# Kernel optimization log

Measured on AMD Instinct MI355X. Metric: run time of the kernel, lower is better.

## Reference

```python
import jax, jax.numpy as jnp
import numpy as np

N, E, F_IN, HID, HEADS, CLS = 50000, 600000, 128, 128, 4, 10
OUT_PER_HEAD = HID // HEADS  # 32
NEG_SLOPE = 0.2
BN_EPS = 1e-5


def _gat_conv(h, src, dst, W, att_src, att_dst, bias, heads, out_dim, concat, num_nodes):
    # h: [N, in]; W: [in, heads*out]; att_*: [heads, out]; src/dst include self-loops
    hp = (h @ W).reshape(num_nodes, heads, out_dim)          # [N, H, D]
    a_s = jnp.sum(hp * att_src[None], axis=-1)               # [N, H]
    a_d = jnp.sum(hp * att_dst[None], axis=-1)               # [N, H]
    alpha = jax.nn.leaky_relu(a_s[src] + a_d[dst], NEG_SLOPE)  # [E, H]
    m = jax.ops.segment_max(alpha, dst, num_segments=num_nodes)
    m = jnp.where(jnp.isfinite(m), m, 0.0)
    ex = jnp.exp(alpha - m[dst])
    denom = jax.ops.segment_sum(ex, dst, num_segments=num_nodes)
    attn = ex / (denom[dst] + 1e-16)                         # segment softmax over dst
    msg = hp[src] * attn[..., None]                          # [E, H, D]
    out = jax.ops.segment_sum(msg, dst, num_segments=num_nodes)  # [N, H, D]
    out = out.reshape(num_nodes, heads * out_dim) if concat else out.mean(axis=1)
    return out + bias


def _bn_eval(x, gamma, beta):
    # eval-mode BatchNorm1d with running_mean=0, running_var=1
    return x * (gamma / jnp.sqrt(1.0 + BN_EPS)) + beta


def setup_inputs() -> dict:
    key = jax.random.key(0)
    ks = jax.random.split(key, 16)
    x = jax.random.normal(ks[0], (N, F_IN), dtype=jnp.float32)
    edge_index = jax.random.randint(ks[1], (2, E), 0, N, dtype=jnp.int64)
    s = 0.1
    return {
        "x": x,
        "edge_index": edge_index,
        "W0": jax.random.normal(ks[2], (F_IN, HID), jnp.float32) * s,
        "as0": jax.random.normal(ks[3], (HEADS, OUT_PER_HEAD), jnp.float32) * s,
        "ad0": jax.random.normal(ks[4], (HEADS, OUT_PER_HEAD), jnp.float32) * s,
        "b0": jnp.zeros((HID,), jnp.float32),
        "g0": jnp.ones((HID,), jnp.float32),
        "be0": jnp.zeros((HID,), jnp.float32),
        "W1": jax.random.normal(ks[5], (HID, HID), jnp.float32) * s,
        "as1": jax.random.normal(ks[6], (HEADS, OUT_PER_HEAD), jnp.float32) * s,
        "ad1": jax.random.normal(ks[7], (HEADS, OUT_PER_HEAD), jnp.float32) * s,
        "b1": jnp.zeros((HID,), jnp.float32),
        "g1": jnp.ones((HID,), jnp.float32),
        "be1": jnp.zeros((HID,), jnp.float32),
        "W2": jax.random.normal(ks[8], (HID, CLS), jnp.float32) * s,
        "as2": jax.random.normal(ks[9], (1, CLS), jnp.float32) * s,
        "ad2": jax.random.normal(ks[10], (1, CLS), jnp.float32) * s,
        "b2": jnp.zeros((CLS,), jnp.float32),
    }


def reference(x, edge_index, W0, as0, ad0, b0, g0, be0,
              W1, as1, ad1, b1, g1, be1, W2, as2, ad2, b2):
    # add self-loops (PyG GATConv default)
    loop = jnp.arange(N, dtype=edge_index.dtype)
    src = jnp.concatenate([edge_index[0], loop])
    dst = jnp.concatenate([edge_index[1], loop])
    h = _gat_conv(x, src, dst, W0, as0, ad0, b0, HEADS, OUT_PER_HEAD, True, N)
    h = jax.nn.elu(_bn_eval(h, g0, be0))
    h = _gat_conv(h, src, dst, W1, as1, ad1, b1, HEADS, OUT_PER_HEAD, True, N)
    h = jax.nn.elu(_bn_eval(h, g1, be1))
    out = _gat_conv(h, src, dst, W2, as2, ad2, b2, 1, CLS, False, N)
    return out
```

## Files before the change

### kernel.cpp

```cpp
#include <hip/hip_runtime.h>
#include <hip/hip_bf16.h>
#include <hip/hip_fp16.h>
#include <math.h>

#define N_NODES 50000
#define N_EDGES 600000
#define E_TOT   (N_EDGES + N_NODES)
#define F       128
#define HEADS   4
#define DHEAD   32
#define CLS     10
#define CLS_PAD 16


__global__ void count_deg(const int* __restrict__ ei, int* __restrict__ deg) {
    int e = blockIdx.x * blockDim.x + threadIdx.x;
    if (e >= E_TOT) return;
    int d = (e < N_EDGES) ? ei[N_EDGES + e] : (e - N_EDGES);
    atomicAdd(&deg[d], 1);
}

#define SCAN_BLOCK 256
#define SCAN_ITEMS 4

__global__ void scan1(const int* __restrict__ deg, int* __restrict__ ptr,
                      int* __restrict__ blockSums, int n) {
    __shared__ int sdata[SCAN_BLOCK];
    int t = threadIdx.x;
    int base = blockIdx.x * (SCAN_BLOCK * SCAN_ITEMS) + t * SCAN_ITEMS;
    int v[SCAN_ITEMS];
    int sum = 0;
    #pragma unroll
    for (int i = 0; i < SCAN_ITEMS; i++) {
        int idx = base + i;
        v[i] = (idx < n) ? deg[idx] : 0;
        sum += v[i];
    }
    sdata[t] = sum;
    __syncthreads();
    for (int off = 1; off < SCAN_BLOCK; off <<= 1) {
        int x = 0;
        if (t >= off) x = sdata[t - off];
        __syncthreads();
        if (t >= off) sdata[t] += x;
        __syncthreads();
    }
    int excl = (t > 0) ? sdata[t - 1] : 0;
    if (t == SCAN_BLOCK - 1) blockSums[blockIdx.x] = sdata[t];
    int run = excl;
    #pragma unroll
    for (int i = 0; i < SCAN_ITEMS; i++) {
        int idx = base + i;
        if (idx < n) ptr[idx] = run;
        run += v[i];
    }
}

__global__ void scan2(int* __restrict__ blockSums, int nb) {
    if (threadIdx.x == 0 && blockIdx.x == 0) {
        int run = 0;
        for (int i = 0; i < nb; i++) { int v = blockSums[i]; blockSums[i] = run; run += v; }
    }
}

__global__ void scan3(int* __restrict__ ptr, const int* __restrict__ blockSums,
                      int* __restrict__ cursor, int n, int total) {
    int i = blockIdx.x * blockDim.x + threadIdx.x;
    if (i < n) {
        int v = ptr[i] + blockSums[i / (SCAN_BLOCK * SCAN_ITEMS)];
        ptr[i] = v;
        cursor[i] = v;
    }
    if (i == 0) ptr[n] = total;
}

__global__ void scatter_edges(const int* __restrict__ ei, int* __restrict__ cursor,
                              int* __restrict__ csr_src) {
    int e = blockIdx.x * blockDim.x + threadIdx.x;
    if (e >= E_TOT) return;
    int s, d;
    if (e < N_EDGES) { s = ei[e]; d = ei[N_EDGES + e]; }
    else             { s = d = e - N_EDGES; }
    int pos = atomicAdd(&cursor[d], 1);
    csr_src[pos] = s;
}


__global__ __launch_bounds__(256) void conv_w(const float* __restrict__ W0,
                                              const float* __restrict__ W1,
                                              __half* __restrict__ Wt0,
                                              __half* __restrict__ Wt1) {
    int idx = blockIdx.x * 256 + threadIdx.x;
    if (idx >= 128 * 128) return;
    int k = idx >> 7, c = idx & 127;
    int e = k ^ ((c & 7) << 3);
    Wt0[c * 128 + e] = __float2half(W0[idx]);
    Wt1[c * 128 + e] = __float2half(W1[idx]);
}


using half8_t  = __attribute__((ext_vector_type(8))) _Float16;
using floatx4  = __attribute__((ext_vector_type(4))) float;

__global__ __launch_bounds__(256) void gemm_att_mfma(const float* __restrict__ A,
                                                     const __half* __restrict__ Wt,
                                                     const float* __restrict__ att_s,
                                                     const float* __restrict__ att_d,
                                                     __half* __restrict__ C,
                                                     float* __restrict__ a_s,
                                                     float* __restrict__ a_d, int nrows) {
    __shared__ _Float16 As[64 * 128];
    __shared__ _Float16 Ws[128 * 128];
    int t = threadIdx.x;
    int row0 = blockIdx.x * 64;

    #pragma unroll
    for (int idx = t; idx < 128 * 128 / 8; idx += 256)
        ((float4*)Ws)[idx] = ((const float4*)Wt)[idx];

    #pragma unroll
    for (int idx = t; idx < 64 * 16; idx += 256) {
        int r = idx >> 4, g = idx & 15;
        float4 v0 = make_float4(0.f, 0.f, 0.f, 0.f), v1 = v0;
        if (row0 + r < nrows) {
            const float4* p = (const float4*)(A + (size_t)(row0 + r) * 128 + g * 8);
            v0 = p[0]; v1 = p[1];
        }
        int gs = g ^ (r & 7);
        union { _Float16 h[8]; float4 f; } u;
        u.h[0] = (_Float16)v0.x; u.h[1] = (_Float16)v0.y;
        u.h[2] = (_Float16)v0.z; u.h[3] = (_Float16)v0.w;
        u.h[4] = (_Float16)v1.x; u.h[5] = (_Float16)v1.y;
        u.h[6] = (_Float16)v1.z; u.h[7] = (_Float16)v1.w;
        *(float4*)&As[r * 128 + (gs << 3)] = u.f;
    }
    __syncthreads();

    int wave = t >> 6, l = t & 63;
    int lr = l & 15, lg = l >> 4;
    int arow = wave * 16 + lr;

    floatx4 acc[8];
    #pragma unroll
    for (int c2 = 0; c2 < 8; c2++) acc[c2] = (floatx4){0.f, 0.f, 0.f, 0.f};

    #pragma unroll
    for (int ks = 0; ks < 4; ks++) {
        int gk = ks * 4 + lg;
        half8_t af = *(const half8_t*)&As[arow * 128 + ((gk ^ (arow & 7)) << 3)];
        #pragma unroll
        for (int c2 = 0; c2 < 8; c2++) {
            int col = c2 * 16 + lr;
            half8_t bf = *(const half8_t*)&Ws[col * 128 + ((gk ^ (col & 7)) << 3)];
            acc[c2] = __builtin_amdgcn_mfma_f32_16x16x32_f16(af, bf, acc[c2], 0, 0, 0);
        }
    }

    #pragma unroll
    for (int c2 = 0; c2 < 8; c2++) {
        int col = c2 * 16 + lr;
        #pragma unroll
        for (int r = 0; r < 4; r++) {
            int row = row0 + wave * 16 + lg * 4 + r;
            if (row < nrows) C[(size_t)row * 128 + col] = __float2half(acc[c2][r]);
        }
    }

    float asv[8], adv8[8];
    #pragma unroll
    for (int c2 = 0; c2 < 8; c2++) {
        asv[c2]  = att_s[c2 * 16 + lr];
        adv8[c2] = att_d[c2 * 16 + lr];
    }
    float ps[4][4], pd[4][4];
    #pragma unroll
    for (int r = 0; r < 4; r++)
        #pragma unroll
        for (int hh = 0; hh < 4; hh++) {
            ps[r][hh] = acc[2 * hh][r] * asv[2 * hh] + acc[2 * hh + 1][r] * asv[2 * hh + 1];
            pd[r][hh] = acc[2 * hh][r] * adv8[2 * hh] + acc[2 * hh + 1][r] * adv8[2 * hh + 1];
        }
    #pragma unroll
    for (int m = 1; m <= 8; m <<= 1) {
        #pragma unroll
        for (int r = 0; r < 4; r++)
            #pragma unroll
            for (int hh = 0; hh < 4; hh++) {
                ps[r][hh] += __shfl_xor(ps[r][hh], m);
                pd[r][hh] += __shfl_xor(pd[r][hh], m);
            }
    }
    if (lr == 0) {
        #pragma unroll
        for (int r = 0; r < 4; r++) {
            int row = row0 + wave * 16 + lg * 4 + r;
            if (row < nrows) {
                *(float4*)(a_s + (size_t)row * 4) = make_float4(ps[r][0], ps[r][1], ps[r][2], ps[r][3]);
                *(float4*)(a_d + (size_t)row * 4) = make_float4(pd[r][0], pd[r][1], pd[r][2], pd[r][3]);
            }
        }
    }
}


__global__ __launch_bounds__(128) void gat_aggr(const __half2* __restrict__ hp,
                                                const float* __restrict__ a_s,
                                                const float* __restrict__ a_d,
                                                const int* __restrict__ ptr,
                                                const int* __restrict__ csr,
                                                const float* __restrict__ bias,
                                                const float* __restrict__ gamma,
                                                const float* __restrict__ beta,
                                                float* __restrict__ out) {
    int t = threadIdx.x;
    int node = blockIdx.x * 2 + (t >> 6);
    int local = t & 63;
    int h = local >> 4;
    int beg = ptr[node], end = ptr[node + 1];
    float adh = a_d[(size_t)node * 4 + h];
    float ax = 0.f, ay = 0.f, l = 0.f;
    int i = beg;
    for (; i + 3 < end; i += 4) {
        int s0 = csr[i], s1 = csr[i + 1], s2 = csr[i + 2], s3 = csr[i + 3];
        float al0 = a_s[(size_t)s0 * 4 + h] + adh;
        float al1 = a_s[(size_t)s1 * 4 + h] + adh;
        float al2 = a_s[(size_t)s2 * 4 + h] + adh;
        float al3 = a_s[(size_t)s3 * 4 + h] + adh;
        al0 = (al0 > 0.f) ? al0 : 0.2f * al0;
        al1 = (al1 > 0.f) ? al1 : 0.2f * al1;
        al2 = (al2 > 0.f) ? al2 : 0.2f * al2;
        al3 = (al3 > 0.f) ? al3 : 0.2f * al3;
        float w0 = __expf(al0), w1 = __expf(al1), w2 = __expf(al2), w3 = __expf(al3);
        float2 v0 = __half22float2(hp[(size_t)s0 * 64 + local]);
        float2 v1 = __half22float2(hp[(size_t)s1 * 64 + local]);
        float2 v2 = __half22float2(hp[(size_t)s2 * 64 + local]);
        float2 v3 = __half22float2(hp[(size_t)s3 * 64 + local]);
        l  += w0 + w1 + w2 + w3;
        ax += w0 * v0.x + w1 * v1.x + w2 * v2.x + w3 * v3.x;
        ay += w0 * v0.y + w1 * v1.y + w2 * v2.y + w3 * v3.y;
    }
    for (; i < end; i++) {
        int s0 = csr[i];
        float al = a_s[(size_t)s0 * 4 + h] + adh;
        al = (al > 0.f) ? al : 0.2f * al;
        float w = __expf(al);
        float2 v = __half22float2(hp[(size_t)s0 * 64 + local]);
        l  += w;
        ax += w * v.x;
        ay += w * v.y;
    }
    float inv = 1.f / (l + 1e-16f);
    int c = local * 2;
    const float rs = rsqrtf(1.f + 1e-5f);
    float vx = ax * inv + bias[c];
    float vy = ay * inv + bias[c + 1];
    vx = vx * (gamma[c] * rs) + beta[c];
    vy = vy * (gamma[c + 1] * rs) + beta[c + 1];
    vx = (vx > 0.f) ? vx : expm1f(vx);
    vy = (vy > 0.f) ? vy : expm1f(vy);
    *(float2*)(out + (size_t)node * 128 + c) = make_float2(vx, vy);
}


__global__ __launch_bounds__(256) void cls_fused(const float* __restrict__ A,
                                                 const float* __restrict__ W2,
                                                 const float* __restrict__ as2,
                                                 const float* __restrict__ ad2,
                                                 float* __restrict__ hp2,
                                                 float* __restrict__ asn,
                                                 float* __restrict__ adn) {
    __shared__ float W2s[128 * CLS];
    __shared__ float av[2 * CLS];
    int t = threadIdx.x;
    for (int idx = t; idx < 128 * CLS; idx += 256) W2s[idx] = W2[idx];
    if (t < CLS) av[t] = as2[t];
    else if (t < 2 * CLS) av[t] = ad2[t - CLS];
    __syncthreads();

    int node = blockIdx.x * 64 + (t >> 2);
    int q = t & 3;
    if (node >= N_NODES) return;
    float acc[CLS];
    #pragma unroll
    for (int c = 0; c < CLS; c++) acc[c] = 0.f;
    const float4* arow = (const float4*)(A + (size_t)node * 128) + q * 8;
    #pragma unroll
    for (int kk = 0; kk < 8; kk++) {
        float4 a = arow[kk];
        int k = q * 32 + kk * 4;
        #pragma unroll
        for (int c = 0; c < CLS; c++) {
            acc[c] += a.x * W2s[(k + 0) * CLS + c] + a.y * W2s[(k + 1) * CLS + c]
                    + a.z * W2s[(k + 2) * CLS + c] + a.w * W2s[(k + 3) * CLS + c];
        }
    }
    #pragma unroll
    for (int c = 0; c < CLS; c++) {
        acc[c] += __shfl_xor(acc[c], 1, 4);
        acc[c] += __shfl_xor(acc[c], 2, 4);
    }
    if (q == 0) {
        float s = 0.f, d = 0.f;
        float* row = hp2 + (size_t)node * CLS_PAD;
        #pragma unroll
        for (int c = 0; c < CLS; c++) {
            row[c] = acc[c];
            s += acc[c] * av[c];
            d += acc[c] * av[CLS + c];
        }
        asn[node] = s;
        adn[node] = d;
    }
}

__global__ __launch_bounds__(256) void gat_aggr2(const float* __restrict__ hp2,
                                                 const float* __restrict__ asn,
                                                 const float* __restrict__ adn,
                                                 const int* __restrict__ ptr,
                                                 const int* __restrict__ csr,
                                                 const float* __restrict__ b2,
                                                 float* __restrict__ out) {
    int gid = blockIdx.x * blockDim.x + threadIdx.x;
    int node = gid >> 4;
    int c = gid & 15;
    if (node >= N_NODES) return;
    int beg = ptr[node], end = ptr[node + 1];
    int cc = (c < CLS) ? c : 0;
    float adv = adn[node];
    float acc = 0.f, l = 0.f;
    int i = beg;
    for (; i + 1 < end; i += 2) {
        int s0 = csr[i], s1 = csr[i + 1];
        float al0 = asn[s0] + adv;
        float al1 = asn[s1] + adv;
        al0 = (al0 > 0.f) ? al0 : 0.2f * al0;
        al1 = (al1 > 0.f) ? al1 : 0.2f * al1;
        float w0 = __expf(al0), w1 = __expf(al1);
        float v0 = hp2[(size_t)s0 * CLS_PAD + cc];
        float v1 = hp2[(size_t)s1 * CLS_PAD + cc];
        l += w0 + w1;
        acc += w0 * v0 + w1 * v1;
    }
    if (i < end) {
        int s0 = csr[i];
        float al = asn[s0] + adv;
        al = (al > 0.f) ? al : 0.2f * al;
        float w = __expf(al);
        l += w;
        acc += w * hp2[(size_t)s0 * CLS_PAD + cc];
    }
    if (c < CLS) out[(size_t)node * CLS + c] = acc / (l + 1e-16f) + b2[c];
}


extern "C" void kernel_launch(void* const* d_in, const int* in_sizes, int n_in,
                              void* d_out, int out_size, void* d_ws, size_t ws_size,
                              hipStream_t stream) {
    const float* x   = (const float*)d_in[0];
    const int*   ei  = (const int*)  d_in[1];
    const float* W0  = (const float*)d_in[2];
    const float* as0 = (const float*)d_in[3];
    const float* ad0 = (const float*)d_in[4];
    const float* b0  = (const float*)d_in[5];
    const float* g0  = (const float*)d_in[6];
    const float* be0 = (const float*)d_in[7];
    const float* W1  = (const float*)d_in[8];
    const float* as1 = (const float*)d_in[9];
    const float* ad1 = (const float*)d_in[10];
    const float* b1  = (const float*)d_in[11];
    const float* g1  = (const float*)d_in[12];
    const float* be1 = (const float*)d_in[13];
    const float* W2  = (const float*)d_in[14];
    const float* as2 = (const float*)d_in[15];
    const float* ad2 = (const float*)d_in[16];
    const float* b2  = (const float*)d_in[17];

    char* ws = (char*)d_ws;
    size_t off = 0;
    auto alloc = [&](size_t bytes) -> void* {
        void* p = ws + off;
        off += (bytes + 255) & ~(size_t)255;
        return p;
    };
    int*    ptr    = (int*)   alloc((N_NODES + 1) * sizeof(int));
    int*    cursor = (int*)   alloc(N_NODES * sizeof(int));
    int*    bsums  = (int*)   alloc(64 * sizeof(int));
    int*    csr    = (int*)   alloc(E_TOT * sizeof(int));
    __half* hp     = (__half*)alloc((size_t)N_NODES * 128 * sizeof(__half));
    float*  hc     = (float*) alloc((size_t)N_NODES * 128 * sizeof(float));
    float*  a_s    = (float*) alloc(N_NODES * 4 * sizeof(float));
    float*  a_d    = (float*) alloc(N_NODES * 4 * sizeof(float));
    float*  hp2    = (float*) alloc((size_t)N_NODES * CLS_PAD * sizeof(float));
    float*  asn    = (float*) alloc(N_NODES * sizeof(float));
    float*  adn    = (float*) alloc(N_NODES * sizeof(float));
    __half* Wt0    = (__half*)alloc(128 * 128 * sizeof(__half));
    __half* Wt1    = (__half*)alloc(128 * 128 * sizeof(__half));

    hipMemsetAsync(cursor, 0, N_NODES * sizeof(int), stream);
    count_deg<<<(E_TOT + 255) / 256, 256, 0, stream>>>(ei, cursor);
    int nScanBlocks = (N_NODES + SCAN_BLOCK * SCAN_ITEMS - 1) / (SCAN_BLOCK * SCAN_ITEMS);
    scan1<<<nScanBlocks, SCAN_BLOCK, 0, stream>>>(cursor, ptr, bsums, N_NODES);
    scan2<<<1, 64, 0, stream>>>(bsums, nScanBlocks);
    scan3<<<(N_NODES + 255) / 256, 256, 0, stream>>>(ptr, bsums, cursor, N_NODES, E_TOT);
    scatter_edges<<<(E_TOT + 255) / 256, 256, 0, stream>>>(ei, cursor, csr);

    conv_w<<<64, 256, 0, stream>>>(W0, W1, Wt0, Wt1);

    int gemmBlocks = (N_NODES + 63) / 64;

    gemm_att_mfma<<<gemmBlocks, 256, 0, stream>>>(x, Wt0, as0, ad0, hp, a_s, a_d, N_NODES);
    gat_aggr<<<N_NODES / 2, 128, 0, stream>>>((const __half2*)hp, a_s, a_d, ptr, csr,
                                              b0, g0, be0, hc);

    gemm_att_mfma<<<gemmBlocks, 256, 0, stream>>>(hc, Wt1, as1, ad1, hp, a_s, a_d, N_NODES);
    gat_aggr<<<N_NODES / 2, 128, 0, stream>>>((const __half2*)hp, a_s, a_d, ptr, csr,
                                              b1, g1, be1, hc);

    cls_fused<<<(N_NODES + 63) / 64, 256, 0, stream>>>(hc, W2, as2, ad2, hp2, asn, adn);
    gat_aggr2<<<(N_NODES * 16 + 255) / 256, 256, 0, stream>>>(hp2, asn, adn, ptr, csr, b2,
                                                              (float*)d_out);
}
```

Measured before the change: 321.8 us.

## Store hidden activations in fp16, process two edges per wave, place self-loops in scan

Hidden-layer activations between layers are now stored as fp16 instead of fp32, so the GEMM and classifier kernels read half-precision inputs directly. The aggregation kernel splits each wave into two edge slots, each lane handling four channels with 8-byte loads, and combines the slots with a shuffle. Self-loops are written into the CSR during the scan instead of going through the atomic scatter. The GEMM swaps MFMA operands so each lane writes contiguous packed fp16 output, and the attention-dot reduction is restructured. The extra fp16 rounding of intermediates adds a small accuracy risk.

```diff
diff --git a/kernel.cpp b/kernel.cpp
--- a/kernel.cpp
+++ b/kernel.cpp
@@ -15,9 +15,8 @@
 
 __global__ void count_deg(const int* __restrict__ ei, int* __restrict__ deg) {
     int e = blockIdx.x * blockDim.x + threadIdx.x;
-    if (e >= E_TOT) return;
-    int d = (e < N_EDGES) ? ei[N_EDGES + e] : (e - N_EDGES);
-    atomicAdd(&deg[d], 1);
+    if (e >= N_EDGES) return;
+    atomicAdd(&deg[ei[N_EDGES + e]], 1);
 }
 
 #define SCAN_BLOCK 256
@@ -33,7 +32,7 @@
     #pragma unroll
     for (int i = 0; i < SCAN_ITEMS; i++) {
         int idx = base + i;
-        v[i] = (idx < n) ? deg[idx] : 0;
+        v[i] = (idx < n) ? (deg[idx] + 1) : 0;
         sum += v[i];
     }
     sdata[t] = sum;
@@ -64,12 +63,13 @@
 }
 
 __global__ void scan3(int* __restrict__ ptr, const int* __restrict__ blockSums,
-                      int* __restrict__ cursor, int n, int total) {
+                      int* __restrict__ cursor, int* __restrict__ csr, int n, int total) {
     int i = blockIdx.x * blockDim.x + threadIdx.x;
     if (i < n) {
         int v = ptr[i] + blockSums[i / (SCAN_BLOCK * SCAN_ITEMS)];
         ptr[i] = v;
-        cursor[i] = v;
+        cursor[i] = v + 1;
+        csr[v] = i;
     }
     if (i == 0) ptr[n] = total;
 }
@@ -77,10 +77,8 @@
 __global__ void scatter_edges(const int* __restrict__ ei, int* __restrict__ cursor,
                               int* __restrict__ csr_src) {
     int e = blockIdx.x * blockDim.x + threadIdx.x;
-    if (e >= E_TOT) return;
-    int s, d;
-    if (e < N_EDGES) { s = ei[e]; d = ei[N_EDGES + e]; }
-    else             { s = d = e - N_EDGES; }
+    if (e >= N_EDGES) return;
+    int s = ei[e], d = ei[N_EDGES + e];
     int pos = atomicAdd(&cursor[d], 1);
     csr_src[pos] = s;
 }
@@ -102,7 +100,8 @@
 using half8_t  = __attribute__((ext_vector_type(8))) _Float16;
 using floatx4  = __attribute__((ext_vector_type(4))) float;
 
-__global__ __launch_bounds__(256) void gemm_att_mfma(const float* __restrict__ A,
+template<bool HALF_IN>
+__global__ __launch_bounds__(256) void gemm_att_mfma(const void* __restrict__ Ain,
                                                      const __half* __restrict__ Wt,
                                                      const float* __restrict__ att_s,
                                                      const float* __restrict__ att_d,
@@ -118,21 +117,35 @@
     for (int idx = t; idx < 128 * 128 / 8; idx += 256)
         ((float4*)Ws)[idx] = ((const float4*)Wt)[idx];
 
-    #pragma unroll
-    for (int idx = t; idx < 64 * 16; idx += 256) {
-        int r = idx >> 4, g = idx & 15;
-        float4 v0 = make_float4(0.f, 0.f, 0.f, 0.f), v1 = v0;
-        if (row0 + r < nrows) {
-            const float4* p = (const float4*)(A + (size_t)(row0 + r) * 128 + g * 8);
-            v0 = p[0]; v1 = p[1];
-        }
-        int gs = g ^ (r & 7);
-        union { _Float16 h[8]; float4 f; } u;
-        u.h[0] = (_Float16)v0.x; u.h[1] = (_Float16)v0.y;
-        u.h[2] = (_Float16)v0.z; u.h[3] = (_Float16)v0.w;
-        u.h[4] = (_Float16)v1.x; u.h[5] = (_Float16)v1.y;
-        u.h[6] = (_Float16)v1.z; u.h[7] = (_Float16)v1.w;
-        *(float4*)&As[r * 128 + (gs << 3)] = u.f;
+    if constexpr (HALF_IN) {
+        const __half* A = (const __half*)Ain;
+        #pragma unroll
+        for (int idx = t; idx < 64 * 16; idx += 256) {
+            int r = idx >> 4, g = idx & 15;
+            float4 v = make_float4(0.f, 0.f, 0.f, 0.f);
+            if (row0 + r < nrows)
+                v = *(const float4*)(A + (size_t)(row0 + r) * 128 + g * 8);
+            int gs = g ^ (r & 7);
+            *(float4*)&As[r * 128 + (gs << 3)] = v;
+        }
+    } else {
+        const float* A = (const float*)Ain;
+        #pragma unroll
+        for (int idx = t; idx < 64 * 16; idx += 256) {
+            int r = idx >> 4, g = idx & 15;
+            float4 v0 = make_float4(0.f, 0.f, 0.f, 0.f), v1 = v0;
+            if (row0 + r < nrows) {
+                const float4* p = (const float4*)(A + (size_t)(row0 + r) * 128 + g * 8);
+                v0 = p[0]; v1 = p[1];
+            }
+            int gs = g ^ (r & 7);
+            union { _Float16 h[8]; float4 f; } u;
+            u.h[0] = (_Float16)v0.x; u.h[1] = (_Float16)v0.y;
+            u.h[2] = (_Float16)v0.z; u.h[3] = (_Float16)v0.w;
+            u.h[4] = (_Float16)v1.x; u.h[5] = (_Float16)v1.y;
+            u.h[6] = (_Float16)v1.z; u.h[7] = (_Float16)v1.w;
+            *(float4*)&As[r * 128 + (gs << 3)] = u.f;
+        }
     }
     __syncthreads();
 
@@ -152,58 +165,47 @@
         for (int c2 = 0; c2 < 8; c2++) {
             int col = c2 * 16 + lr;
             half8_t bf = *(const half8_t*)&Ws[col * 128 + ((gk ^ (col & 7)) << 3)];
-            acc[c2] = __builtin_amdgcn_mfma_f32_16x16x32_f16(af, bf, acc[c2], 0, 0, 0);
-        }
-    }
+            acc[c2] = __builtin_amdgcn_mfma_f32_16x16x32_f16(bf, af, acc[c2], 0, 0, 0);
+        }
+    }
+
+    int row = row0 + arow;
+    bool rowOk = row < nrows;
 
     #pragma unroll
     for (int c2 = 0; c2 < 8; c2++) {
-        int col = c2 * 16 + lr;
+        __half2 p0 = __floats2half2_rn(acc[c2][0], acc[c2][1]);
+        __half2 p1 = __floats2half2_rn(acc[c2][2], acc[c2][3]);
+        uint2 u;
+        u.x = *(unsigned*)&p0;
+        u.y = *(unsigned*)&p1;
+        if (rowOk) ((uint2*)C)[(size_t)row * 32 + c2 * 4 + lg] = u;
+    }
+
+    float ps[4] = {0.f, 0.f, 0.f, 0.f}, pd[4] = {0.f, 0.f, 0.f, 0.f};
+    #pragma unroll
+    for (int c2 = 0; c2 < 8; c2++) {
         #pragma unroll
         for (int r = 0; r < 4; r++) {
-            int row = row0 + wave * 16 + lg * 4 + r;
-            if (row < nrows) C[(size_t)row * 128 + col] = __float2half(acc[c2][r]);
-        }
-    }
-
-    float asv[8], adv8[8];
-    #pragma unroll
-    for (int c2 = 0; c2 < 8; c2++) {
-        asv[c2]  = att_s[c2 * 16 + lr];
-        adv8[c2] = att_d[c2 * 16 + lr];
-    }
-    float ps[4][4], pd[4][4];
-    #pragma unroll
-    for (int r = 0; r < 4; r++)
-        #pragma unroll
-        for (int hh = 0; hh < 4; hh++) {
-            ps[r][hh] = acc[2 * hh][r] * asv[2 * hh] + acc[2 * hh + 1][r] * asv[2 * hh + 1];
-            pd[r][hh] = acc[2 * hh][r] * adv8[2 * hh] + acc[2 * hh + 1][r] * adv8[2 * hh + 1];
-        }
-    #pragma unroll
-    for (int m = 1; m <= 8; m <<= 1) {
-        #pragma unroll
-        for (int r = 0; r < 4; r++)
-            #pragma unroll
-            for (int hh = 0; hh < 4; hh++) {
-                ps[r][hh] += __shfl_xor(ps[r][hh], m);
-                pd[r][hh] += __shfl_xor(pd[r][hh], m);
-            }
-    }
-    if (lr == 0) {
-        #pragma unroll
-        for (int r = 0; r < 4; r++) {
-            int row = row0 + wave * 16 + lg * 4 + r;
-            if (row < nrows) {
-                *(float4*)(a_s + (size_t)row * 4) = make_float4(ps[r][0], ps[r][1], ps[r][2], ps[r][3]);
-                *(float4*)(a_d + (size_t)row * 4) = make_float4(pd[r][0], pd[r][1], pd[r][2], pd[r][3]);
-            }
-        }
-    }
-}
-
-
-__global__ __launch_bounds__(128) void gat_aggr(const __half2* __restrict__ hp,
+            int col = c2 * 16 + lg * 4 + r;
+            float v = acc[c2][r];
+            ps[c2 >> 1] += v * att_s[col];
+            pd[c2 >> 1] += v * att_d[col];
+        }
+    }
+    #pragma unroll
+    for (int hh = 0; hh < 4; hh++) {
+        ps[hh] += __shfl_xor(ps[hh], 16); ps[hh] += __shfl_xor(ps[hh], 32);
+        pd[hh] += __shfl_xor(pd[hh], 16); pd[hh] += __shfl_xor(pd[hh], 32);
+    }
+    if (lg == 0 && rowOk) {
+        *(float4*)(a_s + (size_t)row * 4) = make_float4(ps[0], ps[1], ps[2], ps[3]);
+        *(float4*)(a_d + (size_t)row * 4) = make_float4(pd[0], pd[1], pd[2], pd[3]);
+    }
+}
+
+
+__global__ __launch_bounds__(128) void gat_aggr(const uint2* __restrict__ hp,
                                                 const float* __restrict__ a_s,
                                                 const float* __restrict__ a_d,
                                                 const int* __restrict__ ptr,
@@ -211,58 +213,58 @@
                                                 const float* __restrict__ bias,
                                                 const float* __restrict__ gamma,
                                                 const float* __restrict__ beta,
-                                                float* __restrict__ out) {
+                                                __half* __restrict__ out) {
     int t = threadIdx.x;
     int node = blockIdx.x * 2 + (t >> 6);
-    int local = t & 63;
-    int h = local >> 4;
+    int lane = t & 63;
+    int eslot = lane >> 5;
+    int lc = lane & 31;
+    int h = lc >> 3;
     int beg = ptr[node], end = ptr[node + 1];
     float adh = a_d[(size_t)node * 4 + h];
-    float ax = 0.f, ay = 0.f, l = 0.f;
-    int i = beg;
-    for (; i + 3 < end; i += 4) {
-        int s0 = csr[i], s1 = csr[i + 1], s2 = csr[i + 2], s3 = csr[i + 3];
-        float al0 = a_s[(size_t)s0 * 4 + h] + adh;
-        float al1 = a_s[(size_t)s1 * 4 + h] + adh;
-        float al2 = a_s[(size_t)s2 * 4 + h] + adh;
-        float al3 = a_s[(size_t)s3 * 4 + h] + adh;
-        al0 = (al0 > 0.f) ? al0 : 0.2f * al0;
-        al1 = (al1 > 0.f) ? al1 : 0.2f * al1;
-        al2 = (al2 > 0.f) ? al2 : 0.2f * al2;
-        al3 = (al3 > 0.f) ? al3 : 0.2f * al3;
-        float w0 = __expf(al0), w1 = __expf(al1), w2 = __expf(al2), w3 = __expf(al3);
-        float2 v0 = __half22float2(hp[(size_t)s0 * 64 + local]);
-        float2 v1 = __half22float2(hp[(size_t)s1 * 64 + local]);
-        float2 v2 = __half22float2(hp[(size_t)s2 * 64 + local]);
-        float2 v3 = __half22float2(hp[(size_t)s3 * 64 + local]);
-        l  += w0 + w1 + w2 + w3;
-        ax += w0 * v0.x + w1 * v1.x + w2 * v2.x + w3 * v3.x;
-        ay += w0 * v0.y + w1 * v1.y + w2 * v2.y + w3 * v3.y;
-    }
-    for (; i < end; i++) {
-        int s0 = csr[i];
-        float al = a_s[(size_t)s0 * 4 + h] + adh;
-        al = (al > 0.f) ? al : 0.2f * al;
-        float w = __expf(al);
-        float2 v = __half22float2(hp[(size_t)s0 * 64 + local]);
-        l  += w;
-        ax += w * v.x;
-        ay += w * v.y;
-    }
-    float inv = 1.f / (l + 1e-16f);
-    int c = local * 2;
-    const float rs = rsqrtf(1.f + 1e-5f);
-    float vx = ax * inv + bias[c];
-    float vy = ay * inv + bias[c + 1];
-    vx = vx * (gamma[c] * rs) + beta[c];
-    vy = vy * (gamma[c + 1] * rs) + beta[c + 1];
-    vx = (vx > 0.f) ? vx : expm1f(vx);
-    vy = (vy > 0.f) ? vy : expm1f(vy);
-    *(float2*)(out + (size_t)node * 128 + c) = make_float2(vx, vy);
-}
-
-
-__global__ __launch_bounds__(256) void cls_fused(const float* __restrict__ A,
+    float a0 = 0.f, a1 = 0.f, a2 = 0.f, a3 = 0.f, l = 0.f;
+    for (int i = beg; i < end; i += 4) {
+        #pragma unroll
+        for (int p = 0; p < 2; p++) {
+            int idx = i + p * 2 + eslot;
+            bool valid = idx < end;
+            int s = valid ? csr[idx] : 0;
+            float al = a_s[(size_t)s * 4 + h] + adh;
+            al = (al > 0.f) ? al : 0.2f * al;
+            float w = valid ? __expf(al) : 0.f;
+            uint2 raw = hp[(size_t)s * 32 + lc];
+            float2 f01 = __half22float2(*(__half2*)&raw.x);
+            float2 f23 = __half22float2(*(__half2*)&raw.y);
+            l  += w;
+            a0 += w * f01.x; a1 += w * f01.y;
+            a2 += w * f23.x; a3 += w * f23.y;
+        }
+    }
+    l  += __shfl_xor(l, 32);
+    a0 += __shfl_xor(a0, 32); a1 += __shfl_xor(a1, 32);
+    a2 += __shfl_xor(a2, 32); a3 += __shfl_xor(a3, 32);
+    if (eslot == 0) {
+        float inv = 1.f / (l + 1e-16f);
+        int c = lc * 4;
+        const float rs = rsqrtf(1.f + 1e-5f);
+        float4 bs = *(const float4*)(bias + c);
+        float4 gm = *(const float4*)(gamma + c);
+        float4 bt = *(const float4*)(beta + c);
+        float v0 = a0 * inv + bs.x; v0 = v0 * (gm.x * rs) + bt.x; v0 = (v0 > 0.f) ? v0 : expm1f(v0);
+        float v1 = a1 * inv + bs.y; v1 = v1 * (gm.y * rs) + bt.y; v1 = (v1 > 0.f) ? v1 : expm1f(v1);
+        float v2 = a2 * inv + bs.z; v2 = v2 * (gm.z * rs) + bt.z; v2 = (v2 > 0.f) ? v2 : expm1f(v2);
+        float v3 = a3 * inv + bs.w; v3 = v3 * (gm.w * rs) + bt.w; v3 = (v3 > 0.f) ? v3 : expm1f(v3);
+        __half2 p0 = __floats2half2_rn(v0, v1);
+        __half2 p1 = __floats2half2_rn(v2, v3);
+        uint2 u;
+        u.x = *(unsigned*)&p0;
+        u.y = *(unsigned*)&p1;
+        ((uint2*)out)[(size_t)node * 32 + lc] = u;
+    }
+}
+
+
+__global__ __launch_bounds__(256) void cls_fused(const __half* __restrict__ A,
                                                  const float* __restrict__ W2,
                                                  const float* __restrict__ as2,
                                                  const float* __restrict__ ad2,
@@ -283,15 +285,18 @@
     float acc[CLS];
     #pragma unroll
     for (int c = 0; c < CLS; c++) acc[c] = 0.f;
-    const float4* arow = (const float4*)(A + (size_t)node * 128) + q * 8;
-    #pragma unroll
-    for (int kk = 0; kk < 8; kk++) {
-        float4 a = arow[kk];
-        int k = q * 32 + kk * 4;
-        #pragma unroll
-        for (int c = 0; c < CLS; c++) {
-            acc[c] += a.x * W2s[(k + 0) * CLS + c] + a.y * W2s[(k + 1) * CLS + c]
-                    + a.z * W2s[(k + 2) * CLS + c] + a.w * W2s[(k + 3) * CLS + c];
+    const float4* arow = (const float4*)(A + (size_t)node * 128 + q * 32);
+    #pragma unroll
+    for (int kk = 0; kk < 4; kk++) {
+        float4 raw = arow[kk];
+        __half2* hh = (__half2*)&raw;
+        #pragma unroll
+        for (int j = 0; j < 4; j++) {
+            float2 f = __half22float2(hh[j]);
+            int k = q * 32 + kk * 8 + j * 2;
+            #pragma unroll
+            for (int c = 0; c < CLS; c++)
+                acc[c] += f.x * W2s[k * CLS + c] + f.y * W2s[(k + 1) * CLS + c];
         }
     }
     #pragma unroll
@@ -328,26 +333,19 @@
     int cc = (c < CLS) ? c : 0;
     float adv = adn[node];
     float acc = 0.f, l = 0.f;
-    int i = beg;
-    for (; i + 1 < end; i += 2) {
-        int s0 = csr[i], s1 = csr[i + 1];
-        float al0 = asn[s0] + adv;
-        float al1 = asn[s1] + adv;
-        al0 = (al0 > 0.f) ? al0 : 0.2f * al0;
-        al1 = (al1 > 0.f) ? al1 : 0.2f * al1;
-        float w0 = __expf(al0), w1 = __expf(al1);
-        float v0 = hp2[(size_t)s0 * CLS_PAD + cc];
-        float v1 = hp2[(size_t)s1 * CLS_PAD + cc];
-        l += w0 + w1;
-        acc += w0 * v0 + w1 * v1;
-    }
-    if (i < end) {
-        int s0 = csr[i];
-        float al = asn[s0] + adv;
-        al = (al > 0.f) ? al : 0.2f * al;
-        float w = __expf(al);
-        l += w;
-        acc += w * hp2[(size_t)s0 * CLS_PAD + cc];
+    for (int i = beg; i < end; i += 4) {
+        #pragma unroll
+        for (int p = 0; p < 4; p++) {
+            int idx = i + p;
+            bool valid = idx < end;
+            int s = valid ? csr[idx] : 0;
+            float al = asn[s] + adv;
+            al = (al > 0.f) ? al : 0.2f * al;
+            float w = valid ? __expf(al) : 0.f;
+            float v = hp2[(size_t)s * CLS_PAD + cc];
+            l += w;
+            acc += w * v;
+        }
     }
     if (c < CLS) out[(size_t)node * CLS + c] = acc / (l + 1e-16f) + b2[c];
 }
@@ -387,7 +385,7 @@
     int*    bsums  = (int*)   alloc(64 * sizeof(int));
     int*    csr    = (int*)   alloc(E_TOT * sizeof(int));
     __half* hp     = (__half*)alloc((size_t)N_NODES * 128 * sizeof(__half));
-    float*  hc     = (float*) alloc((size_t)N_NODES * 128 * sizeof(float));
+    __half* hc     = (__half*)alloc((size_t)N_NODES * 128 * sizeof(__half));
     float*  a_s    = (float*) alloc(N_NODES * 4 * sizeof(float));
     float*  a_d    = (float*) alloc(N_NODES * 4 * sizeof(float));
     float*  hp2    = (float*) alloc((size_t)N_NODES * CLS_PAD * sizeof(float));
@@ -397,23 +395,23 @@
     __half* Wt1    = (__half*)alloc(128 * 128 * sizeof(__half));
 
     hipMemsetAsync(cursor, 0, N_NODES * sizeof(int), stream);
-    count_deg<<<(E_TOT + 255) / 256, 256, 0, stream>>>(ei, cursor);
+    count_deg<<<(N_EDGES + 255) / 256, 256, 0, stream>>>(ei, cursor);
     int nScanBlocks = (N_NODES + SCAN_BLOCK * SCAN_ITEMS - 1) / (SCAN_BLOCK * SCAN_ITEMS);
     scan1<<<nScanBlocks, SCAN_BLOCK, 0, stream>>>(cursor, ptr, bsums, N_NODES);
     scan2<<<1, 64, 0, stream>>>(bsums, nScanBlocks);
-    scan3<<<(N_NODES + 255) / 256, 256, 0, stream>>>(ptr, bsums, cursor, N_NODES, E_TOT);
-    scatter_edges<<<(E_TOT + 255) / 256, 256, 0, stream>>>(ei, cursor, csr);
+    scan3<<<(N_NODES + 255) / 256, 256, 0, stream>>>(ptr, bsums, cursor, csr, N_NODES, E_TOT);
+    scatter_edges<<<(N_EDGES + 255) / 256, 256, 0, stream>>>(ei, cursor, csr);
 
     conv_w<<<64, 256, 0, stream>>>(W0, W1, Wt0, Wt1);
 
     int gemmBlocks = (N_NODES + 63) / 64;
 
-    gemm_att_mfma<<<gemmBlocks, 256, 0, stream>>>(x, Wt0, as0, ad0, hp, a_s, a_d, N_NODES);
-    gat_aggr<<<N_NODES / 2, 128, 0, stream>>>((const __half2*)hp, a_s, a_d, ptr, csr,
+    gemm_att_mfma<false><<<gemmBlocks, 256, 0, stream>>>(x, Wt0, as0, ad0, hp, a_s, a_d, N_NODES);
+    gat_aggr<<<N_NODES / 2, 128, 0, stream>>>((const uint2*)hp, a_s, a_d, ptr, csr,
                                               b0, g0, be0, hc);
 
-    gemm_att_mfma<<<gemmBlocks, 256, 0, stream>>>(hc, Wt1, as1, ad1, hp, a_s, a_d, N_NODES);
-    gat_aggr<<<N_NODES / 2, 128, 0, stream>>>((const __half2*)hp, a_s, a_d, ptr, csr,
+    gemm_att_mfma<true><<<gemmBlocks, 256, 0, stream>>>(hc, Wt1, as1, ad1, hp, a_s, a_d, N_NODES);
+    gat_aggr<<<N_NODES / 2, 128, 0, stream>>>((const uint2*)hp, a_s, a_d, ptr, csr,
                                               b1, g1, be1, hc);
 
     cls_fused<<<(N_NODES + 63) / 64, 256, 0, stream>>>(hc, W2, as2, ad2, hp2, asn, adn);
```

After: 357.2 us. 1.11x slower.
